# Kernel optimization log

Hardware: AMD Instinct MI355X
Metric: run time of the kernel (lower is better)

The kernel has to match this reference:

```python
import jax, jax.numpy as jnp
import numpy as np

H = 768
W = 768
N = 64


def setup_inputs() -> dict:
    key = jax.random.key(0)
    k1, k2, k3 = jax.random.split(key, 3)
    img = jax.random.normal(k1, (H, W, 3), dtype=jnp.float32)
    # control points lie inside the image
    pi = jax.random.uniform(k2, (N, 2), dtype=jnp.float32, minval=0.0, maxval=float(min(W, H)))
    qi = pi + 20.0 * jax.random.normal(k3, (N, 2), dtype=jnp.float32)
    return {"img": img, "pi": pi, "qi": qi}


def reference(img, pi, qi):
    # MLS rigid deformation (Schaefer et al.). Returns dense remap grid (H, W, 2).
    h, w = img.shape[0], img.shape[1]
    n = pi.shape[0]
    pi = pi.astype(jnp.float32)
    qi = qi.astype(jnp.float32)

    # v[x, y] = (x, y); matches torch coordinate_buffer[0:W, 0:H]
    xs = jnp.arange(w, dtype=jnp.float32)
    ys = jnp.arange(h, dtype=jnp.float32)
    v = jnp.stack(jnp.meshgrid(xs, ys, indexing="ij"), axis=-1)  # (W, H, 2)

    # inverse-square-distance weights, (W, H, N)
    d2 = jnp.sum((pi[None, None, :, :] - v[:, :, None, :]) ** 2, axis=-1)
    wgt = 1.0 / (d2 + 1e-9)
    sw = jnp.sum(wgt, axis=2, keepdims=True)  # (W, H, 1)

    pstar = jnp.matmul(wgt, pi) / sw  # (W, H, 2) weighted centroid of pi
    qstar = jnp.matmul(wgt, qi) / sw  # (W, H, 2) weighted centroid of qi

    phat = pi[None, None, :, :] - pstar[:, :, None, :]  # (W, H, N, 2)
    qhat = qi[None, None, :, :] - qstar[:, :, None, :]  # (W, H, N, 2)

    vp = v - pstar  # (W, H, 2)
    vp_perp = jnp.stack((vp[..., 1], -vp[..., 0]), axis=-1)            # (W, H, 2)
    phat_perp = jnp.stack((phat[..., 1], -phat[..., 0]), axis=-1)      # (W, H, N, 2)

    # Entries of the 2x2 similarity blocks A_n = w_n * [[a, b], [c, d]] computed
    # as fused contractions instead of materializing (W, H, N, 2, 2).
    a = jnp.einsum("whnc,whc->whn", phat, vp)
    b = jnp.einsum("whnc,whc->whn", phat, vp_perp)
    c = jnp.einsum("whnc,whc->whn", phat_perp, vp)
    d = jnp.einsum("whnc,whc->whn", phat_perp, vp_perp)

    # frv = sum_n qhat_n (1x2) @ A_n (2x2)
    frv_x = jnp.sum(wgt * (qhat[..., 0] * a + qhat[..., 1] * c), axis=2)
    frv_y = jnp.sum(wgt * (qhat[..., 0] * b + qhat[..., 1] * d), axis=2)
    frv = jnp.stack((frv_x, frv_y), axis=-1)  # (W, H, 2)

    vp_norm = jnp.linalg.norm(vp, axis=-1, keepdims=True)          # (W, H, 1)
    frv_norm = jnp.linalg.norm(frv, axis=-1, keepdims=True) + 1e-10
    fv = vp_norm * frv / frv_norm + qstar                           # (W, H, 2)

    return jnp.transpose(fv, (1, 0, 2))  # (H, W, 2)
```

## Files before the change

kernel.cpp:

```cpp
#include <hip/hip_runtime.h>


#define IMG_H 768
#define IMG_W 768
#define NPTS 64

__global__ __launch_bounds__(256, 8) void mls_main(
    const float* __restrict__ pi,
    const float* __restrict__ qi,
    float* __restrict__ out)
{
    const int idx = blockIdx.x * 256 + threadIdx.x;
    const int x = idx % IMG_W;
    const int y = idx / IMG_W;
    const float vx = (float)x;
    const float vy = (float)y;

    float sw = 0.f, spx = 0.f, spy = 0.f;
    float sqx = 0.f, sqy = 0.f, sre = 0.f, sim = 0.f;

    #pragma unroll
    for (int n = 0; n < NPTS; ++n) {
        const float px = pi[2 * n + 0];
        const float py = pi[2 * n + 1];
        const float qx = qi[2 * n + 0];
        const float qy = qi[2 * n + 1];

        const float dx = px - vx;
        const float dy = py - vy;
        const float t  = fmaf(dy, dy, 1e-9f);
        const float d0 = fmaf(dx, dx, t);
        const float w  = __builtin_amdgcn_rcpf(d0);

        const float u0 = w * qx;
        const float u1 = w * qy;
        sw  += w;
        spx = fmaf(w,  px, spx);
        spy = fmaf(w,  py, spy);
        sqx += u0;
        sqy += u1;
        sre = fmaf(u0, px, sre);
        sre = fmaf(u1, py, sre);
        sim = fmaf(u1, px, sim);
        sim = fmaf(-u0, py, sim);
    }

    const float rsw = __builtin_amdgcn_rcpf(sw);
    const float psx = spx * rsw, psy = spy * rsw;
    const float qsx = sqx * rsw, qsy = sqy * rsw;
    const float cre = fmaf(sqx, spx, sqy * spy) * rsw;
    const float cim = fmaf(sqy, spx, -sqx * spy) * rsw;
    const float Sre = sre - cre;
    const float Sim = sim - cim;
    const float vpx = vx - psx;
    const float vpy = vy - psy;
    const float frx = fmaf(vpx, Sre, -vpy * Sim);
    const float fry = fmaf(vpx, Sim, vpy * Sre);
    const float vpn = sqrtf(fmaf(vpx, vpx, vpy * vpy));
    const float frn = sqrtf(fmaf(frx, frx, fry * fry)) + 1e-10f;
    const float s = vpn * __builtin_amdgcn_rcpf(frn);

    ((float2*)out)[idx] = make_float2(fmaf(s, frx, qsx), fmaf(s, fry, qsy));
}

extern "C" void kernel_launch(void* const* d_in, const int* in_sizes, int n_in,
                              void* d_out, int out_size, void* d_ws, size_t ws_size,
                              hipStream_t stream) {
    const float* pi = (const float*)d_in[1];
    const float* qi = (const float*)d_in[2];
    float* out = (float*)d_out;

    const int npix = IMG_H * IMG_W;
    mls_main<<<npix / 256, 256, 0, stream>>>(pi, qi, out);
}
```

Baseline: 21.35 us.

## Process two horizontally adjacent pixels per thread with packed float2 math

Each thread now computes two neighbouring pixels in a row. The dy term and the control-point loads are shared between them, and the accumulations are written as float2 vector ops so the compiler can emit packed FP32 instructions (v_pk_fma/v_pk_mul). Output is stored as one float4 per thread, and the block size drops to 128 with half as many threads. This aims to cut the per-pixel ALU and scalar-load overhead, at the cost of more registers per thread and fewer waves in flight.

```diff
diff --git a/kernel.cpp b/kernel.cpp
--- a/kernel.cpp
+++ b/kernel.cpp
@@ -1,23 +1,47 @@
 #include <hip/hip_runtime.h>
 
+
+typedef float f2 __attribute__((ext_vector_type(2)));
 
 #define IMG_H 768
 #define IMG_W 768
 #define NPTS 64
 
-__global__ __launch_bounds__(256, 8) void mls_main(
+__device__ __forceinline__ float2 mls_finish(
+    float vxk, float vy, float sw,
+    f2 sp, f2 sq, float sre, float sim)
+{
+    const float rsw = __builtin_amdgcn_rcpf(sw);
+    const float psx = sp.x * rsw, psy = sp.y * rsw;
+    const float qsx = sq.x * rsw, qsy = sq.y * rsw;
+    const float cre = fmaf(sq.x, sp.x, sq.y * sp.y) * rsw;
+    const float cim = fmaf(sq.y, sp.x, -sq.x * sp.y) * rsw;
+    const float Sre = sre - cre;
+    const float Sim = sim - cim;
+    const float vpx = vxk - psx;
+    const float vpy = vy - psy;
+    const float frx = fmaf(vpx, Sre, -vpy * Sim);
+    const float fry = fmaf(vpx, Sim, vpy * Sre);
+    const float vpn = sqrtf(fmaf(vpx, vpx, vpy * vpy));
+    const float frn = sqrtf(fmaf(frx, frx, fry * fry)) + 1e-10f;
+    const float s = vpn * __builtin_amdgcn_rcpf(frn);
+    return make_float2(fmaf(s, frx, qsx), fmaf(s, fry, qsy));
+}
+
+__global__ __launch_bounds__(128) void mls_main(
     const float* __restrict__ pi,
     const float* __restrict__ qi,
     float* __restrict__ out)
 {
-    const int idx = blockIdx.x * 256 + threadIdx.x;
-    const int x = idx % IMG_W;
-    const int y = idx / IMG_W;
-    const float vx = (float)x;
+    const int idx = blockIdx.x * 128 + threadIdx.x;
+    const int xh = idx % (IMG_W / 2);
+    const int y  = idx / (IMG_W / 2);
+    const float vx = (float)(2 * xh);
     const float vy = (float)y;
 
-    float sw = 0.f, spx = 0.f, spy = 0.f;
-    float sqx = 0.f, sqy = 0.f, sre = 0.f, sim = 0.f;
+    f2 sw2 = {0.f, 0.f};
+    f2 sp0 = {0.f, 0.f}, sq0 = {0.f, 0.f}, A0 = {0.f, 0.f}, C0 = {0.f, 0.f};
+    f2 sp1 = {0.f, 0.f}, sq1 = {0.f, 0.f}, A1 = {0.f, 0.f}, C1 = {0.f, 0.f};
 
     #pragma unroll
     for (int n = 0; n < NPTS; ++n) {
@@ -25,42 +49,29 @@
         const float py = pi[2 * n + 1];
         const float qx = qi[2 * n + 0];
         const float qy = qi[2 * n + 1];
+        const f2 ppk = {px, py};
+        const f2 qpk = {qx, qy};
 
         const float dx = px - vx;
         const float dy = py - vy;
         const float t  = fmaf(dy, dy, 1e-9f);
-        const float d0 = fmaf(dx, dx, t);
-        const float w  = __builtin_amdgcn_rcpf(d0);
+        const f2 dd  = {dx, dx - 1.f};
+        const f2 d01 = dd * dd + (f2){t, t};
+        const float w0 = __builtin_amdgcn_rcpf(d01.x);
+        const float w1 = __builtin_amdgcn_rcpf(d01.y);
 
-        const float u0 = w * qx;
-        const float u1 = w * qy;
-        sw  += w;
-        spx = fmaf(w,  px, spx);
-        spy = fmaf(w,  py, spy);
-        sqx += u0;
-        sqy += u1;
-        sre = fmaf(u0, px, sre);
-        sre = fmaf(u1, py, sre);
-        sim = fmaf(u1, px, sim);
-        sim = fmaf(-u0, py, sim);
+        sw2 += (f2){w0, w1};
+        sp0 += w0 * ppk;          sp1 += w1 * ppk;
+        const f2 u0 = w0 * qpk;   const f2 u1 = w1 * qpk;
+        sq0 += u0;                sq1 += u1;
+        A0 += u0 * px;            A1 += u1 * px;
+        C0 += u0 * py;            C1 += u1 * py;
     }
 
-    const float rsw = __builtin_amdgcn_rcpf(sw);
-    const float psx = spx * rsw, psy = spy * rsw;
-    const float qsx = sqx * rsw, qsy = sqy * rsw;
-    const float cre = fmaf(sqx, spx, sqy * spy) * rsw;
-    const float cim = fmaf(sqy, spx, -sqx * spy) * rsw;
-    const float Sre = sre - cre;
-    const float Sim = sim - cim;
-    const float vpx = vx - psx;
-    const float vpy = vy - psy;
-    const float frx = fmaf(vpx, Sre, -vpy * Sim);
-    const float fry = fmaf(vpx, Sim, vpy * Sre);
-    const float vpn = sqrtf(fmaf(vpx, vpx, vpy * vpy));
-    const float frn = sqrtf(fmaf(frx, frx, fry * fry)) + 1e-10f;
-    const float s = vpn * __builtin_amdgcn_rcpf(frn);
+    const float2 r0 = mls_finish(vx,       vy, sw2.x, sp0, sq0, A0.x + C0.y, A0.y - C0.x);
+    const float2 r1 = mls_finish(vx + 1.f, vy, sw2.y, sp1, sq1, A1.x + C1.y, A1.y - C1.x);
 
-    ((float2*)out)[idx] = make_float2(fmaf(s, frx, qsx), fmaf(s, fry, qsy));
+    ((float4*)out)[idx] = make_float4(r0.x, r0.y, r1.x, r1.y);
 }
 
 extern "C" void kernel_launch(void* const* d_in, const int* in_sizes, int n_in,
@@ -70,6 +81,6 @@
     const float* qi = (const float*)d_in[2];
     float* out = (float*)d_out;
 
-    const int npix = IMG_H * IMG_W;
-    mls_main<<<npix / 256, 256, 0, stream>>>(pi, qi, out);
+    const int nthreads = IMG_H * (IMG_W / 2);
+    mls_main<<<nthreads / 128, 128, 0, stream>>>(pi, qi, out);
 }
```

New measurement: 19.41 us. -9.1%, faster.
